# Performance work log

Hardware: AMD Instinct MI355X
Metric: run time of the kernel (lower is better)

Reference implementation:

```python
import jax, jax.numpy as jnp
import numpy as np

NUM_HEADS = 12
HEAD_DIM = 64  # hidden_size 768 / 12 heads


def setup_inputs() -> dict:
    key = jax.random.key(0)
    ks = jax.random.split(key, 9)
    B, S, D = 64, 577, 768
    s = 0.02
    return {
        "hidden_states": jax.random.normal(ks[0], (B, S, D), jnp.float32),
        "Wq": jax.random.normal(ks[1], (D, D), jnp.float32) * s,
        "bq": jax.random.normal(ks[2], (D,), jnp.float32) * s,
        "Wk": jax.random.normal(ks[3], (D, D), jnp.float32) * s,
        "bk": jax.random.normal(ks[4], (D,), jnp.float32) * s,
        "Wv": jax.random.normal(ks[5], (D, D), jnp.float32) * s,
        "bv": jax.random.normal(ks[6], (D,), jnp.float32) * s,
        "Wo": jax.random.normal(ks[7], (D, D), jnp.float32) * s,
        "bo": jax.random.normal(ks[8], (D,), jnp.float32) * s,
    }


def _split_heads(x):
    # [B, S, D] -> [B, H, S, Dh]
    B, S, D = x.shape
    return x.reshape(B, S, NUM_HEADS, HEAD_DIM).transpose(0, 2, 1, 3)


def reference(hidden_states, Wq, bq, Wk, bk, Wv, bv, Wo, bo):
    # LinearSparse forward math == nn.Linear: x @ W.T + b (quantize/masker only
    # alter activations saved for backward, not the forward values).
    q = _split_heads(hidden_states @ Wq.T + bq)  # [B,H,S,Dh]
    k = _split_heads(hidden_states @ Wk.T + bk)
    v = _split_heads(hidden_states @ Wv.T + bv)

    scale = 1.0 / np.sqrt(HEAD_DIM).astype(np.float32)
    scores = jnp.einsum("bhqd,bhkd->bhqk", q, k) * scale  # [B,H,S,S]
    probs = jax.nn.softmax(scores, axis=-1)
    ctx = jnp.einsum("bhqk,bhkd->bhqd", probs, v)  # [B,H,S,Dh]

    B, H, S, Dh = ctx.shape
    ctx = ctx.transpose(0, 2, 1, 3).reshape(B, S, H * Dh)  # [B,S,D]
    out = ctx @ Wo.T + bo  # proj_dropout has rate 0 -> identity
    return out
```

## Files before the change

### kernel.cpp

```cpp
#include <hip/hip_runtime.h>
#include <hip/hip_bf16.h>
#include <cstddef>


using bf16x8 = __attribute__((ext_vector_type(8))) short;
using bf16x4 = __attribute__((ext_vector_type(4))) short;
using f32x4  = __attribute__((ext_vector_type(4))) float;

#define MFMA16(a, b, c) __builtin_amdgcn_mfma_f32_16x16x32_bf16((a), (b), (c), 0, 0, 0)

#define SLEN   577
#define NHEAD  12
#define DMODEL 768
#define SPAD   584
#define NQT    10

static __device__ __forceinline__ bf16x8 zero8() {
    bf16x8 z;
#pragma unroll
    for (int i = 0; i < 8; ++i) z[i] = 0;
    return z;
}

static __device__ __forceinline__ short f2b(float f) {
    return __builtin_bit_cast(short, __float2bfloat16(f));
}

static __device__ __forceinline__ void cp16_async(const __hip_bfloat16* g,
                                                  __hip_bfloat16* l) {
    __builtin_amdgcn_global_load_lds(
        (const __attribute__((address_space(1))) unsigned int*)g,
        (__attribute__((address_space(3))) unsigned int*)l,
        16, 0, 0);
}

__global__ __launch_bounds__(256) void cvt_f32_bf16(
    const float* __restrict__ in, __hip_bfloat16* __restrict__ out, int n8)
{
    int i = blockIdx.x * blockDim.x + threadIdx.x;
    const int stride = gridDim.x * blockDim.x;
    for (; i < n8; i += stride) {
        const float4* p = (const float4*)(in + (size_t)i * 8);
        float4 a = p[0], b = p[1];
        float f[8] = {a.x, a.y, a.z, a.w, b.x, b.y, b.z, b.w};
        bf16x8 o;
#pragma unroll
        for (int j = 0; j < 8; ++j) o[j] = f2b(f[j]);
        *(bf16x8*)(out + (size_t)i * 8) = o;
    }
}

template <int OMODE>
__global__ __launch_bounds__(256) void gemm128_bt(
    const __hip_bfloat16* __restrict__ A,
    const __hip_bfloat16* __restrict__ W,
    const float* __restrict__ bias,
    void* __restrict__ Cout,
    int M, int N, int K)
{
    __shared__ __hip_bfloat16 As[128][32];
    __shared__ __hip_bfloat16 Bs[128][32];

    const int tid  = threadIdx.x;
    const int lane = tid & 63;
    const int wave = tid >> 6;
    const int wm   = (wave >> 1) * 64;
    const int wn   = (wave & 1) * 64;
    const int quad = lane >> 4;
    const int low  = lane & 15;
    const int m0   = blockIdx.x * 128;
    const int n0   = blockIdx.y * 128;

    const int srow = lane >> 2;
    const int scol = (lane & 3) * 8;

    const int ar0 = m0 + wave * 16 + srow;
    const int ar1 = ar0 + 64;
    const __hip_bfloat16* Ag0 = A + (size_t)(ar0 < M ? ar0 : M - 1) * K + scol;
    const __hip_bfloat16* Ag1 = A + (size_t)(ar1 < M ? ar1 : M - 1) * K + scol;
    const __hip_bfloat16* Bg0 = W + (size_t)(n0 + wave * 16 + srow) * K + scol;
    const __hip_bfloat16* Bg1 = Bg0 + (size_t)64 * K;
    __hip_bfloat16* La0 = &As[wave * 16][0];
    __hip_bfloat16* La1 = &As[64 + wave * 16][0];
    __hip_bfloat16* Lb0 = &Bs[wave * 16][0];
    __hip_bfloat16* Lb1 = &Bs[64 + wave * 16][0];

    f32x4 acc[4][4] = {};

    for (int k0 = 0; k0 < K; k0 += 32) {
        cp16_async(Ag0 + k0, La0);
        cp16_async(Ag1 + k0, La1);
        cp16_async(Bg0 + k0, Lb0);
        cp16_async(Bg1 + k0, Lb1);
        __syncthreads();

        bf16x8 af[4], bfv[4];
#pragma unroll
        for (int i = 0; i < 4; ++i)
            af[i] = *(const bf16x8*)&As[wm + i * 16 + low][quad * 8];
#pragma unroll
        for (int j = 0; j < 4; ++j)
            bfv[j] = *(const bf16x8*)&Bs[wn + j * 16 + low][quad * 8];
#pragma unroll
        for (int i = 0; i < 4; ++i)
#pragma unroll
            for (int j = 0; j < 4; ++j)
                acc[i][j] = MFMA16(af[i], bfv[j], acc[i][j]);
        __syncthreads();
    }

#pragma unroll
    for (int j = 0; j < 4; ++j) {
        const int col = n0 + wn + j * 16 + low;
        const float bv = bias[col];
#pragma unroll
        for (int i = 0; i < 4; ++i) {
#pragma unroll
            for (int r = 0; r < 4; ++r) {
                const int row = m0 + wm + i * 16 + quad * 4 + r;
                if (row < M) {
                    const float v = acc[i][j][r] + bv;
                    if constexpr (OMODE == 0) {
                        ((__hip_bfloat16*)Cout)[(size_t)row * N + col] =
                            __float2bfloat16(v);
                    } else if constexpr (OMODE == 1) {
                        ((float*)Cout)[(size_t)row * N + col] = v;
                    } else {
                        const int b = row / SLEN;
                        const int s = row - b * SLEN;
                        ((__hip_bfloat16*)Cout)
                            [((size_t)b * DMODEL + col) * SPAD + s] =
                            __float2bfloat16(v);
                    }
                }
            }
        }
    }
}

__global__ __launch_bounds__(256) void attn_kernel(
    const __hip_bfloat16* __restrict__ Q,
    const __hip_bfloat16* __restrict__ Kk,
    const __hip_bfloat16* __restrict__ VT,
    __hip_bfloat16* __restrict__ O)
{
    const int bid = blockIdx.x;
    const int w   = (bid & 7) * 960 + (bid >> 3);
    const int bh  = w / NQT;
    const int q0  = (w - bh * NQT) * 64;
    const int b   = bh / NHEAD;
    const int h   = bh - b * NHEAD;
    const int tid  = threadIdx.x;
    const int lane = tid & 63;
    const int wave = tid >> 6;
    const int quad = lane >> 4;
    const int low  = lane & 15;

    __shared__ __hip_bfloat16 Ks[64][72];
    __shared__ __hip_bfloat16 Vt[64][72];
    __shared__ __hip_bfloat16 Ps[4][16][72];

    const size_t base   = (size_t)b * SLEN * DMODEL + (size_t)h * 64;
    const size_t vtbase = (size_t)bh * 64 * SPAD;

    const int qrow = q0 + wave * 16 + low;
    bf16x8 qf0 = zero8(), qf1 = zero8();
    if (qrow < SLEN) {
        qf0 = *(const bf16x8*)(Q + base + (size_t)qrow * DMODEL + quad * 8);
        qf1 = *(const bf16x8*)(Q + base + (size_t)qrow * DMODEL + 32 + quad * 8);
    }

    f32x4 acc[4] = {};
    float m_run = -1e30f;
    float l_run = 0.f;

    const int srow = tid >> 2;
    const int sc   = (tid & 3) * 16;

    for (int c0 = 0; c0 < SLEN; c0 += 64) {
        __syncthreads();
        {
            const int kg = c0 + srow;
            bf16x8 k0v = zero8(), k1v = zero8();
            if (kg < SLEN) {
                const __hip_bfloat16* p = Kk + base + (size_t)kg * DMODEL + sc;
                k0v = *(const bf16x8*)p;
                k1v = *(const bf16x8*)(p + 8);
            }
            *(bf16x8*)&Ks[srow][sc]     = k0v;
            *(bf16x8*)&Ks[srow][sc + 8] = k1v;
        }
        {
            const __hip_bfloat16* p = VT + vtbase + (size_t)srow * SPAD + c0 + sc;
            bf16x8 v0, v1;
            if (c0 + sc + 15 < SLEN) {
                v0 = *(const bf16x8*)p;
                v1 = *(const bf16x8*)(p + 8);
            } else {
                v0 = zero8(); v1 = zero8();
#pragma unroll
                for (int j = 0; j < 8; ++j) {
                    if (c0 + sc + j < SLEN)
                        v0[j] = __builtin_bit_cast(short, p[j]);
                    if (c0 + sc + 8 + j < SLEN)
                        v1[j] = __builtin_bit_cast(short, p[8 + j]);
                }
            }
            *(bf16x8*)&Vt[srow][sc]     = v0;
            *(bf16x8*)&Vt[srow][sc + 8] = v1;
        }
        __syncthreads();

        f32x4 st[4] = {};
#pragma unroll
        for (int t = 0; t < 4; ++t) {
            bf16x8 kf0 = *(const bf16x8*)&Ks[t * 16 + low][quad * 8];
            bf16x8 kf1 = *(const bf16x8*)&Ks[t * 16 + low][32 + quad * 8];
            st[t] = MFMA16(kf0, qf0, st[t]);
            st[t] = MFMA16(kf1, qf1, st[t]);
        }
#pragma unroll
        for (int t = 0; t < 4; ++t) {
#pragma unroll
            for (int r = 0; r < 4; ++r) {
                const bool valid = (c0 + t * 16 + quad * 4 + r) < SLEN;
                const float s = st[t][r] * 0.125f;
                st[t][r] = valid ? s : -1e30f;
            }
        }

        float m0v = fmaxf(fmaxf(st[0][0], st[0][1]), fmaxf(st[0][2], st[0][3]));
        float m1v = fmaxf(fmaxf(st[1][0], st[1][1]), fmaxf(st[1][2], st[1][3]));
        float m2v = fmaxf(fmaxf(st[2][0], st[2][1]), fmaxf(st[2][2], st[2][3]));
        float m3v = fmaxf(fmaxf(st[3][0], st[3][1]), fmaxf(st[3][2], st[3][3]));
        float mx  = fmaxf(fmaxf(m0v, m1v), fmaxf(m2v, m3v));
        mx = fmaxf(mx, __shfl_xor(mx, 16));
        mx = fmaxf(mx, __shfl_xor(mx, 32));

        const float mnew  = fmaxf(m_run, mx);
        const float alpha = __expf(m_run - mnew);
        m_run = mnew;

        float ps = 0.f;
#pragma unroll
        for (int t = 0; t < 4; ++t) {
            bf16x4 pk;
#pragma unroll
            for (int r = 0; r < 4; ++r) {
                const float p = __expf(st[t][r] - mnew);
                ps += p;
                pk[r] = f2b(p);
            }
            *(bf16x4*)&Ps[wave][low][t * 16 + quad * 4] = pk;
        }
        ps += __shfl_xor(ps, 16);
        ps += __shfl_xor(ps, 32);
        l_run = l_run * alpha + ps;

        float av[4];
#pragma unroll
        for (int r = 0; r < 4; ++r) av[r] = __shfl(alpha, quad * 4 + r);
#pragma unroll
        for (int dt = 0; dt < 4; ++dt)
#pragma unroll
            for (int r = 0; r < 4; ++r) acc[dt][r] *= av[r];

        bf16x8 pf0 = *(const bf16x8*)&Ps[wave][low][quad * 8];
        bf16x8 pf1 = *(const bf16x8*)&Ps[wave][low][32 + quad * 8];
#pragma unroll
        for (int dt = 0; dt < 4; ++dt) {
            bf16x8 vf0 = *(const bf16x8*)&Vt[dt * 16 + low][quad * 8];
            bf16x8 vf1 = *(const bf16x8*)&Vt[dt * 16 + low][32 + quad * 8];
            acc[dt] = MFMA16(pf0, vf0, acc[dt]);
            acc[dt] = MFMA16(pf1, vf1, acc[dt]);
        }
    }

    float lrow[4];
#pragma unroll
    for (int r = 0; r < 4; ++r) lrow[r] = __shfl(l_run, quad * 4 + r);

#pragma unroll
    for (int r = 0; r < 4; ++r) {
        const int row = q0 + wave * 16 + quad * 4 + r;
        if (row < SLEN) {
            const float inv = 1.0f / lrow[r];
#pragma unroll
            for (int dt = 0; dt < 4; ++dt)
                O[((size_t)b * SLEN + row) * DMODEL + h * 64 + dt * 16 + low] =
                    __float2bfloat16(acc[dt][r] * inv);
        }
    }
}

extern "C" void kernel_launch(void* const* d_in, const int* in_sizes, int n_in,
                              void* d_out, int out_size, void* d_ws, size_t ws_size,
                              hipStream_t stream) {
    const float* X  = (const float*)d_in[0];
    const float* Wq = (const float*)d_in[1];
    const float* bq = (const float*)d_in[2];
    const float* Wk = (const float*)d_in[3];
    const float* bk = (const float*)d_in[4];
    const float* Wv = (const float*)d_in[5];
    const float* bv = (const float*)d_in[6];
    const float* Wo = (const float*)d_in[7];
    const float* bo = (const float*)d_in[8];

    const int Bb = 64, S = SLEN, D = DMODEL;
    const int M = Bb * S;
    const size_t szX  = (size_t)M * D;
    const size_t szW  = (size_t)D * D;

    __hip_bfloat16* Xb  = (__hip_bfloat16*)d_ws;
    __hip_bfloat16* Wqb = Xb + szX;
    __hip_bfloat16* Wkb = Wqb + szW;
    __hip_bfloat16* Wvb = Wkb + szW;
    __hip_bfloat16* Wob = Wvb + szW;
    __hip_bfloat16* Qb  = Wob + szW;
    __hip_bfloat16* Kb  = Qb + szX;
    __hip_bfloat16* VTb = Kb + szX;
    __hip_bfloat16* Cx  = Xb;
    float* out = (float*)d_out;

    dim3 blk(256);
    cvt_f32_bf16<<<2048, blk, 0, stream>>>(X, Xb, (int)(szX / 8));
    cvt_f32_bf16<<<288,  blk, 0, stream>>>(Wq, Wqb, (int)(szW / 8));
    cvt_f32_bf16<<<288,  blk, 0, stream>>>(Wk, Wkb, (int)(szW / 8));
    cvt_f32_bf16<<<288,  blk, 0, stream>>>(Wv, Wvb, (int)(szW / 8));
    cvt_f32_bf16<<<288,  blk, 0, stream>>>(Wo, Wob, (int)(szW / 8));

    dim3 gG((M + 127) / 128, D / 128);
    gemm128_bt<0><<<gG, blk, 0, stream>>>(Xb, Wqb, bq, (void*)Qb,  M, D, D);
    gemm128_bt<0><<<gG, blk, 0, stream>>>(Xb, Wkb, bk, (void*)Kb,  M, D, D);
    gemm128_bt<2><<<gG, blk, 0, stream>>>(Xb, Wvb, bv, (void*)VTb, M, D, D);

    attn_kernel<<<dim3(Bb * NHEAD * NQT), blk, 0, stream>>>(Qb, Kb, VTb, Cx);

    gemm128_bt<1><<<gG, blk, 0, stream>>>(Cx, Wob, bo, (void*)out, M, D, D);
}
```

Before: 830.5 us.

## Fuse QKV GEMMs, widen K-tile with swizzled LDS, streamline attention softmax

Merges the three Q/K/V projection GEMMs into one launch with an XCD-aware tile swizzle, doubles the K step to 64 and XOR-swizzles the LDS layout to avoid bank conflicts. In attention, the main loop now covers only the 576 full keys with no masking or bounds checks, and the leftover key is handled separately with scalar dot products. Softmax switches to exp2 with a log2e-folded scale and skips the accumulator rescale when no row max changes. This adds code complexity and a divergent tail path, and the XOR swizzle must match between the async copy and the fragment reads.

```diff
diff --git a/kernel.cpp b/kernel.cpp
--- a/kernel.cpp
+++ b/kernel.cpp
@@ -14,6 +14,7 @@
 #define DMODEL 768
 #define SPAD   584
 #define NQT    10
+#define SCALE2 0.18033688f
 
 static __device__ __forceinline__ bf16x8 zero8() {
     bf16x8 z;
@@ -22,8 +23,17 @@
     return z;
 }
 
+static __device__ __forceinline__ float b2f(short s) {
+    return __bfloat162float(__builtin_bit_cast(__hip_bfloat16, s));
+}
 static __device__ __forceinline__ short f2b(float f) {
     return __builtin_bit_cast(short, __float2bfloat16(f));
+}
+
+static __device__ __forceinline__ int xcd_swizzle(int bid, int nwg) {
+    const int xcd = bid & 7, idx = bid >> 3;
+    const int q = nwg >> 3, r = nwg & 7;
+    return (xcd < r ? xcd * (q + 1) : r * (q + 1) + (xcd - r) * q) + idx;
 }
 
 static __device__ __forceinline__ void cp16_async(const __hip_bfloat16* g,
@@ -50,16 +60,32 @@
     }
 }
 
-template <int OMODE>
-__global__ __launch_bounds__(256) void gemm128_bt(
+template <int MODE>
+__global__ __launch_bounds__(256) void gemm_bk64(
     const __hip_bfloat16* __restrict__ A,
-    const __hip_bfloat16* __restrict__ W,
-    const float* __restrict__ bias,
-    void* __restrict__ Cout,
+    const __hip_bfloat16* __restrict__ W0,
+    const __hip_bfloat16* __restrict__ W1,
+    const __hip_bfloat16* __restrict__ W2,
+    const float* __restrict__ bias0,
+    const float* __restrict__ bias1,
+    const float* __restrict__ bias2,
+    void* __restrict__ O0, void* __restrict__ O1, void* __restrict__ O2,
     int M, int N, int K)
 {
-    __shared__ __hip_bfloat16 As[128][32];
-    __shared__ __hip_bfloat16 Bs[128][32];
+    __shared__ __hip_bfloat16 As[128][64];
+    __shared__ __hip_bfloat16 Bs[128][64];
+
+    const int NSUB = (MODE == 0) ? 3 : 1;
+    const int NT   = N / 128;
+    const int nTot = NT * NSUB;
+    const int id   = xcd_swizzle(blockIdx.x, gridDim.x);
+    const int m0   = (id / nTot) * 128;
+    const int nn   = id % nTot;
+    const int sub  = nn / NT;
+    const int n0   = (nn % NT) * 128;
+    const __hip_bfloat16* W = sub == 0 ? W0 : (sub == 1 ? W1 : W2);
+    const float* bias       = sub == 0 ? bias0 : (sub == 1 ? bias1 : bias2);
+    void* C                 = sub == 0 ? O0 : (sub == 1 ? O1 : O2);
 
     const int tid  = threadIdx.x;
     const int lane = tid & 63;
@@ -68,44 +94,51 @@
     const int wn   = (wave & 1) * 64;
     const int quad = lane >> 4;
     const int low  = lane & 15;
-    const int m0   = blockIdx.x * 128;
-    const int n0   = blockIdx.y * 128;
-
-    const int srow = lane >> 2;
-    const int scol = (lane & 3) * 8;
-
-    const int ar0 = m0 + wave * 16 + srow;
-    const int ar1 = ar0 + 64;
-    const __hip_bfloat16* Ag0 = A + (size_t)(ar0 < M ? ar0 : M - 1) * K + scol;
-    const __hip_bfloat16* Ag1 = A + (size_t)(ar1 < M ? ar1 : M - 1) * K + scol;
-    const __hip_bfloat16* Bg0 = W + (size_t)(n0 + wave * 16 + srow) * K + scol;
-    const __hip_bfloat16* Bg1 = Bg0 + (size_t)64 * K;
-    __hip_bfloat16* La0 = &As[wave * 16][0];
-    __hip_bfloat16* La1 = &As[64 + wave * 16][0];
-    __hip_bfloat16* Lb0 = &Bs[wave * 16][0];
-    __hip_bfloat16* Lb1 = &Bs[64 + wave * 16][0];
+
+    const int g    = lane >> 3;
+    const int swzc = (lane & 7) ^ g;
+
+    const __hip_bfloat16* Ag[4];
+    const __hip_bfloat16* Bg[4];
+    __hip_bfloat16* La[4];
+    __hip_bfloat16* Lb[4];
+#pragma unroll
+    for (int c = 0; c < 4; ++c) {
+        int ra = m0 + c * 32 + wave * 8 + g;
+        if (ra >= M) ra = M - 1;
+        const int rb = n0 + c * 32 + wave * 8 + g;
+        Ag[c] = A + (size_t)ra * K + swzc * 8;
+        Bg[c] = W + (size_t)rb * K + swzc * 8;
+        La[c] = &As[0][0] + c * 2048 + wave * 512;
+        Lb[c] = &Bs[0][0] + c * 2048 + wave * 512;
+    }
 
     f32x4 acc[4][4] = {};
 
-    for (int k0 = 0; k0 < K; k0 += 32) {
-        cp16_async(Ag0 + k0, La0);
-        cp16_async(Ag1 + k0, La1);
-        cp16_async(Bg0 + k0, Lb0);
-        cp16_async(Bg1 + k0, Lb1);
+    for (int k0 = 0; k0 < K; k0 += 64) {
+#pragma unroll
+        for (int c = 0; c < 4; ++c) {
+            cp16_async(Ag[c] + k0, La[c]);
+            cp16_async(Bg[c] + k0, Lb[c]);
+        }
         __syncthreads();
 
-        bf16x8 af[4], bfv[4];
-#pragma unroll
-        for (int i = 0; i < 4; ++i)
-            af[i] = *(const bf16x8*)&As[wm + i * 16 + low][quad * 8];
-#pragma unroll
-        for (int j = 0; j < 4; ++j)
-            bfv[j] = *(const bf16x8*)&Bs[wn + j * 16 + low][quad * 8];
-#pragma unroll
-        for (int i = 0; i < 4; ++i)
+#pragma unroll
+        for (int ks = 0; ks < 2; ++ks) {
+            const int ch = ((quad + ks * 4) ^ (low & 7)) * 8;
+            bf16x8 af[4], bfv[4];
+#pragma unroll
+            for (int i = 0; i < 4; ++i)
+                af[i] = *(const bf16x8*)&As[wm + i * 16 + low][ch];
 #pragma unroll
             for (int j = 0; j < 4; ++j)
-                acc[i][j] = MFMA16(af[i], bfv[j], acc[i][j]);
+                bfv[j] = *(const bf16x8*)&Bs[wn + j * 16 + low][ch];
+#pragma unroll
+            for (int i = 0; i < 4; ++i)
+#pragma unroll
+                for (int j = 0; j < 4; ++j)
+                    acc[i][j] = MFMA16(af[i], bfv[j], acc[i][j]);
+        }
         __syncthreads();
     }
 
@@ -120,17 +153,19 @@
                 const int row = m0 + wm + i * 16 + quad * 4 + r;
                 if (row < M) {
                     const float v = acc[i][j][r] + bv;
-                    if constexpr (OMODE == 0) {
-                        ((__hip_bfloat16*)Cout)[(size_t)row * N + col] =
-                            __float2bfloat16(v);
-                    } else if constexpr (OMODE == 1) {
-                        ((float*)Cout)[(size_t)row * N + col] = v;
+                    if constexpr (MODE == 1) {
+                        ((float*)C)[(size_t)row * N + col] = v;
                     } else {
-                        const int b = row / SLEN;
-                        const int s = row - b * SLEN;
-                        ((__hip_bfloat16*)Cout)
-                            [((size_t)b * DMODEL + col) * SPAD + s] =
-                            __float2bfloat16(v);
+                        if (sub < 2) {
+                            ((__hip_bfloat16*)C)[(size_t)row * N + col] =
+                                __float2bfloat16(v);
+                        } else {
+                            const int bb = row / SLEN;
+                            const int s  = row - bb * SLEN;
+                            ((__hip_bfloat16*)C)
+                                [((size_t)bb * DMODEL + col) * SPAD + s] =
+                                __float2bfloat16(v);
+                        }
                     }
                 }
             }
@@ -177,37 +212,15 @@
     const int srow = tid >> 2;
     const int sc   = (tid & 3) * 16;
 
-    for (int c0 = 0; c0 < SLEN; c0 += 64) {
+    for (int c0 = 0; c0 < 576; c0 += 64) {
         __syncthreads();
         {
-            const int kg = c0 + srow;
-            bf16x8 k0v = zero8(), k1v = zero8();
-            if (kg < SLEN) {
-                const __hip_bfloat16* p = Kk + base + (size_t)kg * DMODEL + sc;
-                k0v = *(const bf16x8*)p;
-                k1v = *(const bf16x8*)(p + 8);
-            }
-            *(bf16x8*)&Ks[srow][sc]     = k0v;
-            *(bf16x8*)&Ks[srow][sc + 8] = k1v;
-        }
-        {
-            const __hip_bfloat16* p = VT + vtbase + (size_t)srow * SPAD + c0 + sc;
-            bf16x8 v0, v1;
-            if (c0 + sc + 15 < SLEN) {
-                v0 = *(const bf16x8*)p;
-                v1 = *(const bf16x8*)(p + 8);
-            } else {
-                v0 = zero8(); v1 = zero8();
-#pragma unroll
-                for (int j = 0; j < 8; ++j) {
-                    if (c0 + sc + j < SLEN)
-                        v0[j] = __builtin_bit_cast(short, p[j]);
-                    if (c0 + sc + 8 + j < SLEN)
-                        v1[j] = __builtin_bit_cast(short, p[8 + j]);
-                }
-            }
-            *(bf16x8*)&Vt[srow][sc]     = v0;
-            *(bf16x8*)&Vt[srow][sc + 8] = v1;
+            const __hip_bfloat16* kp = Kk + base + (size_t)(c0 + srow) * DMODEL + sc;
+            *(bf16x8*)&Ks[srow][sc]     = *(const bf16x8*)kp;
+            *(bf16x8*)&Ks[srow][sc + 8] = *(const bf16x8*)(kp + 8);
+            const __hip_bfloat16* vp = VT + vtbase + (size_t)srow * SPAD + c0 + sc;
+            *(bf16x8*)&Vt[srow][sc]     = *(const bf16x8*)vp;
+            *(bf16x8*)&Vt[srow][sc + 8] = *(const bf16x8*)(vp + 8);
         }
         __syncthreads();
 
@@ -220,14 +233,10 @@
             st[t] = MFMA16(kf1, qf1, st[t]);
         }
 #pragma unroll
-        for (int t = 0; t < 4; ++t) {
-#pragma unroll
-            for (int r = 0; r < 4; ++r) {
-                const bool valid = (c0 + t * 16 + quad * 4 + r) < SLEN;
-                const float s = st[t][r] * 0.125f;
-                st[t][r] = valid ? s : -1e30f;
-            }
-        }
+        for (int t = 0; t < 4; ++t)
+#pragma unroll
+            for (int r = 0; r < 4; ++r)
+                st[t][r] *= SCALE2;
 
         float m0v = fmaxf(fmaxf(st[0][0], st[0][1]), fmaxf(st[0][2], st[0][3]));
         float m1v = fmaxf(fmaxf(st[1][0], st[1][1]), fmaxf(st[1][2], st[1][3]));
@@ -237,9 +246,19 @@
         mx = fmaxf(mx, __shfl_xor(mx, 16));
         mx = fmaxf(mx, __shfl_xor(mx, 32));
 
-        const float mnew  = fmaxf(m_run, mx);
-        const float alpha = __expf(m_run - mnew);
-        m_run = mnew;
+        if (__any(mx > m_run)) {
+            const float mnew  = fmaxf(m_run, mx);
+            const float alpha = exp2f(m_run - mnew);
+            m_run = mnew;
+            l_run *= alpha;
+            float av[4];
+#pragma unroll
+            for (int r = 0; r < 4; ++r) av[r] = __shfl(alpha, quad * 4 + r);
+#pragma unroll
+            for (int dt = 0; dt < 4; ++dt)
+#pragma unroll
+                for (int r = 0; r < 4; ++r) acc[dt][r] *= av[r];
+        }
 
         float ps = 0.f;
 #pragma unroll
@@ -247,7 +266,7 @@
             bf16x4 pk;
 #pragma unroll
             for (int r = 0; r < 4; ++r) {
-                const float p = __expf(st[t][r] - mnew);
+                const float p = exp2f(st[t][r] - m_run);
                 ps += p;
                 pk[r] = f2b(p);
             }
@@ -255,15 +274,7 @@
         }
         ps += __shfl_xor(ps, 16);
         ps += __shfl_xor(ps, 32);
-        l_run = l_run * alpha + ps;
-
-        float av[4];
-#pragma unroll
-        for (int r = 0; r < 4; ++r) av[r] = __shfl(alpha, quad * 4 + r);
-#pragma unroll
-        for (int dt = 0; dt < 4; ++dt)
-#pragma unroll
-            for (int r = 0; r < 4; ++r) acc[dt][r] *= av[r];
+        l_run += ps;
 
         bf16x8 pf0 = *(const bf16x8*)&Ps[wave][low][quad * 8];
         bf16x8 pf1 = *(const bf16x8*)&Ps[wave][low][32 + quad * 8];
@@ -273,6 +284,44 @@
             bf16x8 vf1 = *(const bf16x8*)&Vt[dt * 16 + low][32 + quad * 8];
             acc[dt] = MFMA16(pf0, vf0, acc[dt]);
             acc[dt] = MFMA16(pf1, vf1, acc[dt]);
+        }
+    }
+
+    {
+        const __hip_bfloat16* kp = Kk + base + (size_t)576 * DMODEL;
+        bf16x8 k0 = *(const bf16x8*)(kp + quad * 8);
+        bf16x8 k1 = *(const bf16x8*)(kp + 32 + quad * 8);
+        float d = 0.f;
+#pragma unroll
+        for (int j = 0; j < 8; ++j)
+            d += b2f(qf0[j]) * b2f(k0[j]) + b2f(qf1[j]) * b2f(k1[j]);
+        d += __shfl_xor(d, 16);
+        d += __shfl_xor(d, 32);
+        const float s = d * SCALE2;
+        if (__any(s > m_run)) {
+            const float mnew  = fmaxf(m_run, s);
+            const float alpha = exp2f(m_run - mnew);
+            m_run = mnew;
+            l_run *= alpha;
+            float av[4];
+#pragma unroll
+            for (int r = 0; r < 4; ++r) av[r] = __shfl(alpha, quad * 4 + r);
+#pragma unroll
+            for (int dt = 0; dt < 4; ++dt)
+#pragma unroll
+                for (int r = 0; r < 4; ++r) acc[dt][r] *= av[r];
+        }
+        const float p = exp2f(s - m_run);
+        l_run += p;
+        float pq[4];
+#pragma unroll
+        for (int r = 0; r < 4; ++r) pq[r] = __shfl(p, quad * 4 + r);
+#pragma unroll
+        for (int dt = 0; dt < 4; ++dt) {
+            const float vv = __bfloat162float(
+                VT[vtbase + (size_t)(dt * 16 + low) * SPAD + 576]);
+#pragma unroll
+            for (int r = 0; r < 4; ++r) acc[dt][r] += pq[r] * vv;
         }
     }
 
@@ -329,12 +378,14 @@
     cvt_f32_bf16<<<288,  blk, 0, stream>>>(Wv, Wvb, (int)(szW / 8));
     cvt_f32_bf16<<<288,  blk, 0, stream>>>(Wo, Wob, (int)(szW / 8));
 
-    dim3 gG((M + 127) / 128, D / 128);
-    gemm128_bt<0><<<gG, blk, 0, stream>>>(Xb, Wqb, bq, (void*)Qb,  M, D, D);
-    gemm128_bt<0><<<gG, blk, 0, stream>>>(Xb, Wkb, bk, (void*)Kb,  M, D, D);
-    gemm128_bt<2><<<gG, blk, 0, stream>>>(Xb, Wvb, bv, (void*)VTb, M, D, D);
+    const int mTiles = (M + 127) / 128;
+    gemm_bk64<0><<<dim3(mTiles * 18), blk, 0, stream>>>(
+        Xb, Wqb, Wkb, Wvb, bq, bk, bv,
+        (void*)Qb, (void*)Kb, (void*)VTb, M, D, D);
 
     attn_kernel<<<dim3(Bb * NHEAD * NQT), blk, 0, stream>>>(Qb, Kb, VTb, Cx);
 
-    gemm128_bt<1><<<gG, blk, 0, stream>>>(Cx, Wob, bo, (void*)out, M, D, D);
-}
+    gemm_bk64<1><<<dim3(mTiles * 6), blk, 0, stream>>>(
+        Cx, Wob, Wob, Wob, bo, bo, bo,
+        (void*)out, (void*)out, (void*)out, M, D, D);
+}
```

Measured after the change: 744.8 us. 10.3% less time.
